# Kernel optimization log

Measured on AMD Instinct MI355X. Metric: run time of the kernel, lower is better.

## Reference

```python
import jax, jax.numpy as jnp
import numpy as np

B, C, H, W = 8, 1152, 32, 32
N = H * W


def _skew(t):
    # t: (B,3) -> (B,3,3) skew-symmetric
    z = jnp.zeros_like(t[:, 0])
    return jnp.stack([
        jnp.stack([z, -t[:, 2], t[:, 1]], axis=-1),
        jnp.stack([t[:, 2], z, -t[:, 0]], axis=-1),
        jnp.stack([-t[:, 1], t[:, 0], z], axis=-1),
    ], axis=1)


def _fundamental(K1, K2, R, t):
    E = _skew(t) @ R
    U, S, Vt = jnp.linalg.svd(E)
    S = S.at[:, 2].set(0.0)  # enforce rank-2 essential matrix
    E = U @ (S[:, :, None] * Vt)
    return jnp.linalg.inv(jnp.swapaxes(K2, 1, 2)) @ E @ jnp.linalg.inv(K1)


def setup_inputs() -> dict:
    key = jax.random.key(0)
    k1, k2, k3, k4, k5 = jax.random.split(key, 5)
    f_tar = jax.random.normal(k1, (B, C, H, W), dtype=jnp.float32)
    f_src = jax.random.normal(k2, (B, C, H, W), dtype=jnp.float32)
    # realistic invertible intrinsics: [[fx,0,cx],[0,fy,cy],[0,0,1]]
    def intrinsics(k):
        f = 30.0 + 2.0 * jax.random.uniform(k, (B, 2))
        Kt = jnp.zeros((B, 3, 3))
        Kt = Kt.at[:, 0, 0].set(f[:, 0]).at[:, 1, 1].set(f[:, 1])
        Kt = Kt.at[:, 0, 2].set(W / 2.0).at[:, 1, 2].set(H / 2.0).at[:, 2, 2].set(1.0)
        return Kt.astype(jnp.float32)
    K1 = intrinsics(k3)
    K2 = intrinsics(k4)
    # proper rotation via QR of a random matrix
    ka, kb = jax.random.split(k5)
    Q, Rm = jnp.linalg.qr(jax.random.normal(ka, (B, 3, 3)))
    Q = Q * jnp.sign(jnp.diagonal(Rm, axis1=1, axis2=2))[:, None, :]
    Q = Q * jnp.linalg.det(Q)[:, None, None]  # det = +1
    t = jax.random.normal(kb, (B, 3), dtype=jnp.float32)
    return {"f_tar": f_tar, "f_src": f_src, "K1": K1, "K2": K2,
            "R": Q.astype(jnp.float32), "t": t}


def reference(f_tar, f_src, K1, K2, R, t):
    f_src_flat = f_src.reshape(B, C, N)  # (B,C,N)
    # NOTE: torch code computes A = f_src^T @ f_tar but never uses it (dead code); omitted.

    # homogeneous pixel coords, indexing='ij': x=row index, y=col index
    ix, iy = jnp.meshgrid(jnp.arange(H, dtype=jnp.float32),
                          jnp.arange(W, dtype=jnp.float32), indexing='ij')
    combined = jnp.stack([ix.ravel(), iy.ravel(), jnp.ones(N, jnp.float32)], axis=0)  # (3,N)
    combined = jnp.broadcast_to(combined, (B, 3, N))

    F_mat = _fundamental(K1, K2, R, t)                       # (B,3,3)
    lines = F_mat @ combined                                 # (B,3,N)
    lines = lines / lines[:, 2:3, :]

    ones = jnp.ones((B, 1, N), jnp.float32)
    x0 = jnp.zeros((B, 1, N), jnp.float32)
    y0 = -lines[:, 2:3, :] / lines[:, 1:2, :]
    point_0 = jnp.concatenate([x0, y0, ones], axis=1)        # (B,3,N)
    x1 = jnp.full((B, 1, N), float(W), jnp.float32)
    y1 = -(lines[:, 2:3, :] + lines[:, 0:1, :] * W) / lines[:, 1:2, :]
    point_1 = jnp.concatenate([x1, y1, ones], axis=1)        # (B,3,N)

    # point-to-line distance for every (pixel i, line j) pair -> (B,N,N)
    diff = point_0 - point_1                                 # (B,3,N)
    p = combined[:, :, :, None] - point_0[:, :, None, :]     # (B,3,N,N) via broadcast
    d = diff[:, :, None, :]                                  # (B,3,1,N)
    cross = jnp.stack([
        p[:, 1] * d[:, 2] - p[:, 2] * d[:, 1],
        p[:, 2] * d[:, 0] - p[:, 0] * d[:, 2],
        p[:, 0] * d[:, 1] - p[:, 1] * d[:, 0],
    ], axis=1)                                               # (B,3,N,N)
    cross_norm = jnp.sqrt(jnp.sum(cross * cross, axis=1))    # (B,N,N)
    diff_norm = jnp.linalg.norm(diff, axis=1, keepdims=True) # (B,1,N)
    d_epi = cross_norm / diff_norm                           # (B,N,N)

    thre = 0.1
    weight_map = 1.0 - jax.nn.softmax(5.0 * (d_epi - thre), axis=-1)
    attention_map = jax.nn.softmax(weight_map, axis=1)       # softmax over dim=1, per torch code

    out = jnp.einsum('bij,bjc->bic', attention_map, jnp.swapaxes(f_src_flat, 1, 2))  # (B,N,C)
    return out.reshape(B, C, H, W)
```

## Files before the change

### kernel.cpp

```cpp
#include <hip/hip_runtime.h>
#include <hip/hip_bf16.h>
#include <math.h>

#define Bn 8
#define Cn 1152
#define Nn 1024

typedef short short8 __attribute__((ext_vector_type(8)));
typedef float f32x4 __attribute__((ext_vector_type(4)));

__device__ float g_rmax[Bn * Nn];
__device__ float g_rsuminv[Bn * Nn];
__device__ float g_csum_part[Bn * 8 * Nn];
__device__ unsigned short g_A[(size_t)Bn * Nn * Nn];
__device__ unsigned short g_fb[(size_t)Bn * Cn * Nn];

__device__ inline unsigned short f2bf(float x) {
    __hip_bfloat16 h = __float2bfloat16(x);
    unsigned short u;
    __builtin_memcpy(&u, &h, 2);
    return u;
}

__device__ inline void inv3(const float* M, float* o) {
    float a = M[0], b = M[1], c = M[2];
    float d = M[3], e = M[4], f = M[5];
    float g = M[6], h = M[7], i = M[8];
    float A0 = (e * i - f * h);
    float A1 = -(d * i - f * g);
    float A2 = (d * h - e * g);
    float det = a * A0 + b * A1 + c * A2;
    float inv = 1.0f / det;
    o[0] = A0 * inv;
    o[1] = -(b * i - c * h) * inv;
    o[2] = (b * f - c * e) * inv;
    o[3] = A1 * inv;
    o[4] = (a * i - c * g) * inv;
    o[5] = -(a * f - c * d) * inv;
    o[6] = A2 * inv;
    o[7] = -(a * h - b * g) * inv;
    o[8] = (a * e - b * d) * inv;
}

__device__ inline void mm3(const float* X, const float* Y, float* Z) {
    for (int r = 0; r < 3; r++)
        for (int c = 0; c < 3; c++)
            Z[r * 3 + c] = X[r * 3 + 0] * Y[0 * 3 + c] + X[r * 3 + 1] * Y[1 * 3 + c] +
                           X[r * 3 + 2] * Y[2 * 3 + c];
}

__device__ inline void computeF(const float* K1, const float* K2, const float* R,
                                const float* t, int b, float* F) {
    float t0 = t[b * 3 + 0], t1 = t[b * 3 + 1], t2 = t[b * 3 + 2];
    float S[9] = {0.0f, -t2, t1, t2, 0.0f, -t0, -t1, t0, 0.0f};
    float E[9];
    mm3(S, &R[b * 9], E);
    float iK1[9], iK2[9];
    inv3(&K1[b * 9], iK1);
    inv3(&K2[b * 9], iK2);
    float iK2T[9] = {iK2[0], iK2[3], iK2[6], iK2[1], iK2[4], iK2[7], iK2[2], iK2[5], iK2[8]};
    float T[9];
    mm3(iK2T, E, T);
    mm3(T, iK1, F);
}

__device__ inline float4 zcoef(const float* F, int j) {
    float jx = (float)(j >> 5);
    float jy = (float)(j & 31);
    float l0 = F[0] * jx + F[1] * jy + F[2];
    float l1 = F[3] * jx + F[4] * jy + F[5];
    float l2 = F[6] * jx + F[7] * jy + F[8];
    l0 = l0 / l2;
    l1 = l1 / l2;
    float y0 = -1.0f / l1;
    float y1 = -(1.0f + l0 * 32.0f) / l1;
    float dy = y0 - y1;
    float invn = 1.0f / sqrtf(1024.0f + dy * dy);
    return make_float4(5.0f * dy * invn, 160.0f * invn, 160.0f * y0 * invn, 0.0f);
}

__global__ void rowstats_kernel(const float* __restrict__ K1, const float* __restrict__ K2,
                                const float* __restrict__ R, const float* __restrict__ t) {
    __shared__ float Fs[9];
    __shared__ float4 prm[Nn];
    int lin = blockIdx.x;
    int b = lin & 7;
    int seg = lin >> 3;
    if (threadIdx.x == 0) computeF(K1, K2, R, t, b, Fs);
    __syncthreads();
#pragma unroll
    for (int u = 0; u < 4; u++) {
        int j = threadIdx.x * 4 + u;
        prm[j] = zcoef(Fs, j);
    }
    __syncthreads();
    int wv = threadIdx.x >> 6;
    int lane = threadIdx.x & 63;
#pragma unroll
    for (int rr = 0; rr < 8; rr++) {
        int i = seg * 32 + wv * 8 + rr;
        float ix = (float)(i >> 5), iy = (float)(i & 31);
        float z[16], m = -INFINITY;
#pragma unroll
        for (int k = 0; k < 16; k++) {
            float4 p = prm[lane + k * 64];
            z[k] = fabsf(fmaf(ix, p.x, fmaf(iy, p.y, -p.z))) - 0.5f;
            m = fmaxf(m, z[k]);
        }
#pragma unroll
        for (int o = 32; o > 0; o >>= 1) m = fmaxf(m, __shfl_xor(m, o, 64));
        float s = 0.0f;
#pragma unroll
        for (int k = 0; k < 16; k++) s += __expf(z[k] - m);
#pragma unroll
        for (int o = 32; o > 0; o >>= 1) s += __shfl_xor(s, o, 64);
        if (lane == 0) {
            g_rmax[b * Nn + i] = m;
            g_rsuminv[b * Nn + i] = 1.0f / s;
        }
    }
}

__global__ void colE_kernel(const float* __restrict__ K1, const float* __restrict__ K2,
                            const float* __restrict__ R, const float* __restrict__ t) {
    __shared__ float Fs[9];
    __shared__ float rm[128], rs[128];
    __shared__ float4 pj[64];
    __shared__ float4 red[16][16];
    int lin = blockIdx.x;
    int b = lin & 7;
    int r = lin >> 3;
    int jt = r & 15;
    int it = r >> 4;
    int tt = threadIdx.x;
    if (tt < 128) {
        rm[tt] = g_rmax[b * Nn + it * 128 + tt];
        rs[tt] = g_rsuminv[b * Nn + it * 128 + tt];
    }
    if (tt == 0) computeF(K1, K2, R, t, b, Fs);
    __syncthreads();
    if (tt < 64) pj[tt] = zcoef(Fs, jt * 64 + tt);
    __syncthreads();
    int tcol = tt & 15, trow = tt >> 4;
    int j0 = jt * 64 + tcol * 4;
    float4 p0 = pj[tcol * 4 + 0];
    float4 p1 = pj[tcol * 4 + 1];
    float4 p2 = pj[tcol * 4 + 2];
    float4 p3 = pj[tcol * 4 + 3];
    float4 csum = make_float4(0.f, 0.f, 0.f, 0.f);
#pragma unroll
    for (int k = 0; k < 8; k++) {
        int il = trow + k * 16;
        float rmax = rm[il], rsi = rs[il];
        int i = it * 128 + il;
        float ix = (float)(i >> 5), iy = (float)(i & 31);
        float z0 = fabsf(fmaf(ix, p0.x, fmaf(iy, p0.y, -p0.z))) - 0.5f;
        float z1 = fabsf(fmaf(ix, p1.x, fmaf(iy, p1.y, -p1.z))) - 0.5f;
        float z2 = fabsf(fmaf(ix, p2.x, fmaf(iy, p2.y, -p2.z))) - 0.5f;
        float z3 = fabsf(fmaf(ix, p3.x, fmaf(iy, p3.y, -p3.z))) - 0.5f;
        float E0 = __expf(1.0f - __expf(z0 - rmax) * rsi);
        float E1 = __expf(1.0f - __expf(z1 - rmax) * rsi);
        float E2 = __expf(1.0f - __expf(z2 - rmax) * rsi);
        float E3 = __expf(1.0f - __expf(z3 - rmax) * rsi);
        csum.x += E0; csum.y += E1; csum.z += E2; csum.w += E3;
        ushort4 u;
        u.x = f2bf(E0); u.y = f2bf(E1); u.z = f2bf(E2); u.w = f2bf(E3);
        *(ushort4*)&g_A[((size_t)b * Nn + i) * Nn + j0] = u;
    }
    red[trow][tcol] = csum;
    __syncthreads();
    if (tt < 16) {
        float4 s = red[0][tt];
#pragma unroll
        for (int q = 1; q < 16; q++) {
            float4 p = red[q][tt];
            s.x += p.x; s.y += p.y; s.z += p.z; s.w += p.w;
        }
        *(float4*)&g_csum_part[(b * 8 + it) * Nn + jt * 64 + tt * 4] = s;
    }
}

__global__ void convert_fsrc_kernel(const float* __restrict__ f) {
    int lin = blockIdx.x;
    int b = lin & 7;
    int cg = lin >> 3;
    int j0 = threadIdx.x * 4;
    float4 cs = *(const float4*)&g_csum_part[(b * 8 + 0) * Nn + j0];
#pragma unroll
    for (int it = 1; it < 8; it++) {
        float4 p = *(const float4*)&g_csum_part[(b * 8 + it) * Nn + j0];
        cs.x += p.x; cs.y += p.y; cs.z += p.z; cs.w += p.w;
    }
    float4 inv = make_float4(1.0f / cs.x, 1.0f / cs.y, 1.0f / cs.z, 1.0f / cs.w);
#pragma unroll
    for (int c8 = 0; c8 < 8; c8++) {
        int c = cg * 8 + c8;
        size_t off = ((size_t)b * Cn + c) * Nn + j0;
        float4 v = *(const float4*)(f + off);
        ushort4 u;
        u.x = f2bf(v.x * inv.x);
        u.y = f2bf(v.y * inv.y);
        u.z = f2bf(v.z * inv.z);
        u.w = f2bf(v.w * inv.w);
        *(ushort4*)&g_fb[off] = u;
    }
}

#define BM 128
#define BNc 64
#define BK 32

__launch_bounds__(128) __global__ void gemm_kernel(float* __restrict__ out) {
    __shared__ unsigned short As[2][BM * BK];
    __shared__ unsigned short Bs[2][BNc * BK];
    int lin = blockIdx.x;
    int b = lin & 7;
    int s = lin >> 3;
    int it = s & 7;
    int ct = s >> 3;
    int i0 = it * BM;
    int c0 = ct * BNc;
    int t = threadIdx.x;
    int w = t >> 6, L = t & 63;
    const unsigned short* Ab = g_A + (size_t)b * Nn * Nn + (size_t)i0 * Nn;
    const unsigned short* Fb = g_fb + (size_t)b * Cn * Nn + (size_t)c0 * Nn;

    auto stage = [&](int p, int kt) {
#pragma unroll
        for (int h = 0; h < 4; h++) {
            int chunk = h * 128 + t;
            int rr = chunk >> 2;
            int gq = (chunk & 3) ^ ((rr >> 1) & 3);
            const unsigned short* ga = Ab + (size_t)rr * Nn + kt + gq * 8;
            __builtin_amdgcn_global_load_lds(
                (const __attribute__((address_space(1))) unsigned int*)ga,
                (__attribute__((address_space(3))) unsigned int*)(As[p] + chunk * 8), 16, 0, 0);
        }
#pragma unroll
        for (int h = 0; h < 2; h++) {
            int chunk = h * 128 + t;
            int rr = chunk >> 2;
            int gq = (chunk & 3) ^ ((rr >> 1) & 3);
            const unsigned short* gb = Fb + (size_t)rr * Nn + kt + gq * 8;
            __builtin_amdgcn_global_load_lds(
                (const __attribute__((address_space(1))) unsigned int*)gb,
                (__attribute__((address_space(3))) unsigned int*)(Bs[p] + chunk * 8), 16, 0, 0);
        }
    };

    f32x4 acc[4][4] = {};
    int lrow = L & 15, quad = L >> 4;
    stage(0, 0);
    for (int kt = 0; kt < Nn; kt += BK) {
        int p = (kt >> 5) & 1;
        __syncthreads();
        if (kt + BK < Nn) stage(1 - p, kt + BK);
        short8 af[4], bf[4];
#pragma unroll
        for (int mt = 0; mt < 4; mt++) {
            int rr = w * 64 + mt * 16 + lrow;
            int q = quad ^ ((rr >> 1) & 3);
            af[mt] = *(const short8*)(As[p] + rr * BK + q * 8);
        }
#pragma unroll
        for (int nt = 0; nt < 4; nt++) {
            int cc = nt * 16 + lrow;
            int q = quad ^ ((cc >> 1) & 3);
            bf[nt] = *(const short8*)(Bs[p] + cc * BK + q * 8);
        }
#pragma unroll
        for (int mt = 0; mt < 4; mt++)
#pragma unroll
            for (int nt = 0; nt < 4; nt++)
                acc[mt][nt] =
                    __builtin_amdgcn_mfma_f32_16x16x32_bf16(af[mt], bf[nt], acc[mt][nt], 0, 0, 0);
    }
    int col = L & 15;
#pragma unroll
    for (int mt = 0; mt < 4; mt++)
#pragma unroll
        for (int rg = 0; rg < 4; rg++) {
            int i = i0 + w * 64 + mt * 16 + quad * 4 + rg;
            float* orow = out + ((size_t)b * Nn + i) * Cn + c0;
#pragma unroll
            for (int nt = 0; nt < 4; nt++) orow[nt * 16 + col] = acc[mt][nt][rg];
        }
}

extern "C" void kernel_launch(void* const* d_in, const int* in_sizes, int n_in,
                              void* d_out, int out_size, void* d_ws, size_t ws_size,
                              hipStream_t stream) {
    (void)in_sizes; (void)n_in; (void)d_ws; (void)ws_size; (void)out_size;
    const float* f_src = (const float*)d_in[1];
    const float* K1 = (const float*)d_in[2];
    const float* K2 = (const float*)d_in[3];
    const float* R = (const float*)d_in[4];
    const float* t = (const float*)d_in[5];
    float* out = (float*)d_out;

    rowstats_kernel<<<dim3(256), dim3(256), 0, stream>>>(K1, K2, R, t);
    colE_kernel<<<dim3(1024), dim3(256), 0, stream>>>(K1, K2, R, t);
    convert_fsrc_kernel<<<dim3(Bn * Cn / 8), dim3(256), 0, stream>>>(f_src);
    gemm_kernel<<<dim3(Bn * (Nn / BM) * (Cn / BNc)), dim3(128), 0, stream>>>(out);
}
```

Baseline: 170.2 us.

## Fuse row-stats and attention-matrix kernels; enlarge GEMM tile to 128x128

The separate row-softmax statistics and column-exp kernels are merged into one kernel. Each wavefront now computes a row's max and sum and immediately writes the bf16 attention entries, keeping per-lane column partial sums in registers. This removes a kernel launch and the recomputation of the exp terms, but the per-element 2-byte global stores are less vectorised and the column-sum partials grow from 8 to 32 per batch. Separately, the GEMM tile grows from 128x64 with 2 waves to 128x128 with 4 waves, giving more reuse of the A tile and fewer blocks (576 instead of 1152).

```diff
diff --git a/kernel.cpp b/kernel.cpp
--- a/kernel.cpp
+++ b/kernel.cpp
@@ -9,9 +9,7 @@
 typedef short short8 __attribute__((ext_vector_type(8)));
 typedef float f32x4 __attribute__((ext_vector_type(4)));
 
-__device__ float g_rmax[Bn * Nn];
-__device__ float g_rsuminv[Bn * Nn];
-__device__ float g_csum_part[Bn * 8 * Nn];
+__device__ float g_csum_part[Bn * 32 * Nn];
 __device__ unsigned short g_A[(size_t)Bn * Nn * Nn];
 __device__ unsigned short g_fb[(size_t)Bn * Cn * Nn];
 
@@ -79,10 +77,13 @@
     return make_float4(5.0f * dy * invn, 160.0f * invn, 160.0f * y0 * invn, 0.0f);
 }
 
-__global__ void rowstats_kernel(const float* __restrict__ K1, const float* __restrict__ K2,
-                                const float* __restrict__ R, const float* __restrict__ t) {
+__launch_bounds__(256) __global__ void fusedE_kernel(const float* __restrict__ K1,
+                                                     const float* __restrict__ K2,
+                                                     const float* __restrict__ R,
+                                                     const float* __restrict__ t) {
     __shared__ float Fs[9];
     __shared__ float4 prm[Nn];
+    __shared__ float red[4][16][64];
     int lin = blockIdx.x;
     int b = lin & 7;
     int seg = lin >> 3;
@@ -96,87 +97,56 @@
     __syncthreads();
     int wv = threadIdx.x >> 6;
     int lane = threadIdx.x & 63;
+    float px[16], py[16], pz[16];
+#pragma unroll
+    for (int k = 0; k < 16; k++) {
+        float4 p = prm[lane + k * 64];
+        px[k] = p.x;
+        py[k] = p.y;
+        pz[k] = p.z;
+    }
+    float csum[16];
+#pragma unroll
+    for (int k = 0; k < 16; k++) csum[k] = 0.0f;
 #pragma unroll
     for (int rr = 0; rr < 8; rr++) {
         int i = seg * 32 + wv * 8 + rr;
         float ix = (float)(i >> 5), iy = (float)(i & 31);
-        float z[16], m = -INFINITY;
+        float e[16], m = -INFINITY;
 #pragma unroll
         for (int k = 0; k < 16; k++) {
-            float4 p = prm[lane + k * 64];
-            z[k] = fabsf(fmaf(ix, p.x, fmaf(iy, p.y, -p.z))) - 0.5f;
-            m = fmaxf(m, z[k]);
+            e[k] = fabsf(fmaf(ix, px[k], fmaf(iy, py[k], -pz[k]))) - 0.5f;
+            m = fmaxf(m, e[k]);
         }
 #pragma unroll
         for (int o = 32; o > 0; o >>= 1) m = fmaxf(m, __shfl_xor(m, o, 64));
         float s = 0.0f;
 #pragma unroll
-        for (int k = 0; k < 16; k++) s += __expf(z[k] - m);
+        for (int k = 0; k < 16; k++) {
+            e[k] = __expf(e[k] - m);
+            s += e[k];
+        }
 #pragma unroll
         for (int o = 32; o > 0; o >>= 1) s += __shfl_xor(s, o, 64);
-        if (lane == 0) {
-            g_rmax[b * Nn + i] = m;
-            g_rsuminv[b * Nn + i] = 1.0f / s;
-        }
-    }
-}
-
-__global__ void colE_kernel(const float* __restrict__ K1, const float* __restrict__ K2,
-                            const float* __restrict__ R, const float* __restrict__ t) {
-    __shared__ float Fs[9];
-    __shared__ float rm[128], rs[128];
-    __shared__ float4 pj[64];
-    __shared__ float4 red[16][16];
-    int lin = blockIdx.x;
-    int b = lin & 7;
-    int r = lin >> 3;
-    int jt = r & 15;
-    int it = r >> 4;
-    int tt = threadIdx.x;
-    if (tt < 128) {
-        rm[tt] = g_rmax[b * Nn + it * 128 + tt];
-        rs[tt] = g_rsuminv[b * Nn + it * 128 + tt];
-    }
-    if (tt == 0) computeF(K1, K2, R, t, b, Fs);
+        float rsi = 1.0f / s;
+        unsigned short* arow = g_A + (size_t)(b * Nn + i) * Nn;
+#pragma unroll
+        for (int k = 0; k < 16; k++) {
+            float E = __expf(1.0f - e[k] * rsi);
+            csum[k] += E;
+            arow[lane + k * 64] = f2bf(E);
+        }
+    }
+#pragma unroll
+    for (int k = 0; k < 16; k++) red[wv][k][lane] = csum[k];
     __syncthreads();
-    if (tt < 64) pj[tt] = zcoef(Fs, jt * 64 + tt);
-    __syncthreads();
-    int tcol = tt & 15, trow = tt >> 4;
-    int j0 = jt * 64 + tcol * 4;
-    float4 p0 = pj[tcol * 4 + 0];
-    float4 p1 = pj[tcol * 4 + 1];
-    float4 p2 = pj[tcol * 4 + 2];
-    float4 p3 = pj[tcol * 4 + 3];
-    float4 csum = make_float4(0.f, 0.f, 0.f, 0.f);
-#pragma unroll
-    for (int k = 0; k < 8; k++) {
-        int il = trow + k * 16;
-        float rmax = rm[il], rsi = rs[il];
-        int i = it * 128 + il;
-        float ix = (float)(i >> 5), iy = (float)(i & 31);
-        float z0 = fabsf(fmaf(ix, p0.x, fmaf(iy, p0.y, -p0.z))) - 0.5f;
-        float z1 = fabsf(fmaf(ix, p1.x, fmaf(iy, p1.y, -p1.z))) - 0.5f;
-        float z2 = fabsf(fmaf(ix, p2.x, fmaf(iy, p2.y, -p2.z))) - 0.5f;
-        float z3 = fabsf(fmaf(ix, p3.x, fmaf(iy, p3.y, -p3.z))) - 0.5f;
-        float E0 = __expf(1.0f - __expf(z0 - rmax) * rsi);
-        float E1 = __expf(1.0f - __expf(z1 - rmax) * rsi);
-        float E2 = __expf(1.0f - __expf(z2 - rmax) * rsi);
-        float E3 = __expf(1.0f - __expf(z3 - rmax) * rsi);
-        csum.x += E0; csum.y += E1; csum.z += E2; csum.w += E3;
-        ushort4 u;
-        u.x = f2bf(E0); u.y = f2bf(E1); u.z = f2bf(E2); u.w = f2bf(E3);
-        *(ushort4*)&g_A[((size_t)b * Nn + i) * Nn + j0] = u;
-    }
-    red[trow][tcol] = csum;
-    __syncthreads();
-    if (tt < 16) {
-        float4 s = red[0][tt];
-#pragma unroll
-        for (int q = 1; q < 16; q++) {
-            float4 p = red[q][tt];
-            s.x += p.x; s.y += p.y; s.z += p.z; s.w += p.w;
-        }
-        *(float4*)&g_csum_part[(b * 8 + it) * Nn + jt * 64 + tt * 4] = s;
+    int l2 = threadIdx.x & 63;
+    int k0 = (threadIdx.x >> 6) * 4;
+#pragma unroll
+    for (int q = 0; q < 4; q++) {
+        int k = k0 + q;
+        float ssum = red[0][k][l2] + red[1][k][l2] + red[2][k][l2] + red[3][k][l2];
+        g_csum_part[(b * 32 + seg) * Nn + k * 64 + l2] = ssum;
     }
 }
 
@@ -185,10 +155,10 @@
     int b = lin & 7;
     int cg = lin >> 3;
     int j0 = threadIdx.x * 4;
-    float4 cs = *(const float4*)&g_csum_part[(b * 8 + 0) * Nn + j0];
-#pragma unroll
-    for (int it = 1; it < 8; it++) {
-        float4 p = *(const float4*)&g_csum_part[(b * 8 + it) * Nn + j0];
+    float4 cs = *(const float4*)&g_csum_part[(b * 32 + 0) * Nn + j0];
+#pragma unroll
+    for (int it = 1; it < 32; it++) {
+        float4 p = *(const float4*)&g_csum_part[(b * 32 + it) * Nn + j0];
         cs.x += p.x; cs.y += p.y; cs.z += p.z; cs.w += p.w;
     }
     float4 inv = make_float4(1.0f / cs.x, 1.0f / cs.y, 1.0f / cs.z, 1.0f / cs.w);
@@ -207,10 +177,10 @@
 }
 
 #define BM 128
-#define BNc 64
+#define BNc 128
 #define BK 32
 
-__launch_bounds__(128) __global__ void gemm_kernel(float* __restrict__ out) {
+__launch_bounds__(256, 2) __global__ void gemm_kernel(float* __restrict__ out) {
     __shared__ unsigned short As[2][BM * BK];
     __shared__ unsigned short Bs[2][BNc * BK];
     int lin = blockIdx.x;
@@ -222,25 +192,20 @@
     int c0 = ct * BNc;
     int t = threadIdx.x;
     int w = t >> 6, L = t & 63;
+    int wr = w >> 1, wc = w & 1;
     const unsigned short* Ab = g_A + (size_t)b * Nn * Nn + (size_t)i0 * Nn;
     const unsigned short* Fb = g_fb + (size_t)b * Cn * Nn + (size_t)c0 * Nn;
 
     auto stage = [&](int p, int kt) {
 #pragma unroll
-        for (int h = 0; h < 4; h++) {
-            int chunk = h * 128 + t;
+        for (int h = 0; h < 2; h++) {
+            int chunk = h * 256 + t;
             int rr = chunk >> 2;
             int gq = (chunk & 3) ^ ((rr >> 1) & 3);
             const unsigned short* ga = Ab + (size_t)rr * Nn + kt + gq * 8;
             __builtin_amdgcn_global_load_lds(
                 (const __attribute__((address_space(1))) unsigned int*)ga,
                 (__attribute__((address_space(3))) unsigned int*)(As[p] + chunk * 8), 16, 0, 0);
-        }
-#pragma unroll
-        for (int h = 0; h < 2; h++) {
-            int chunk = h * 128 + t;
-            int rr = chunk >> 2;
-            int gq = (chunk & 3) ^ ((rr >> 1) & 3);
             const unsigned short* gb = Fb + (size_t)rr * Nn + kt + gq * 8;
             __builtin_amdgcn_global_load_lds(
                 (const __attribute__((address_space(1))) unsigned int*)gb,
@@ -258,13 +223,13 @@
         short8 af[4], bf[4];
 #pragma unroll
         for (int mt = 0; mt < 4; mt++) {
-            int rr = w * 64 + mt * 16 + lrow;
+            int rr = wr * 64 + mt * 16 + lrow;
             int q = quad ^ ((rr >> 1) & 3);
             af[mt] = *(const short8*)(As[p] + rr * BK + q * 8);
         }
 #pragma unroll
         for (int nt = 0; nt < 4; nt++) {
-            int cc = nt * 16 + lrow;
+            int cc = wc * 64 + nt * 16 + lrow;
             int q = quad ^ ((cc >> 1) & 3);
             bf[nt] = *(const short8*)(Bs[p] + cc * BK + q * 8);
         }
@@ -280,8 +245,8 @@
     for (int mt = 0; mt < 4; mt++)
 #pragma unroll
         for (int rg = 0; rg < 4; rg++) {
-            int i = i0 + w * 64 + mt * 16 + quad * 4 + rg;
-            float* orow = out + ((size_t)b * Nn + i) * Cn + c0;
+            int i = i0 + wr * 64 + mt * 16 + quad * 4 + rg;
+            float* orow = out + ((size_t)b * Nn + i) * Cn + c0 + wc * 64;
 #pragma unroll
             for (int nt = 0; nt < 4; nt++) orow[nt * 16 + col] = acc[mt][nt][rg];
         }
@@ -298,8 +263,7 @@
     const float* t = (const float*)d_in[5];
     float* out = (float*)d_out;
 
-    rowstats_kernel<<<dim3(256), dim3(256), 0, stream>>>(K1, K2, R, t);
-    colE_kernel<<<dim3(1024), dim3(256), 0, stream>>>(K1, K2, R, t);
+    fusedE_kernel<<<dim3(256), dim3(256), 0, stream>>>(K1, K2, R, t);
     convert_fsrc_kernel<<<dim3(Bn * Cn / 8), dim3(256), 0, stream>>>(f_src);
-    gemm_kernel<<<dim3(Bn * (Nn / BM) * (Cn / BNc)), dim3(128), 0, stream>>>(out);
-}
+    gemm_kernel<<<dim3(Bn * (Nn / BM) * (Cn / BNc)), dim3(256), 0, stream>>>(out);
+}
```

Result: faster. 166.6 us (-2.1%).
